# Kernel tuning notes

Measured on AMD Instinct MI355X. Metric: run time of the kernel, lower is better.

## Reference

```python
import jax, jax.numpy as jnp
import numpy as np

N = 2048        # nodes
IN_DIM = 128    # input feature dim
K = 8           # channels
D = 32          # per-channel dim (C_dim)
ITERS = 4       # routing iterations
BETA = 1.0      # attention temperature
EPS = 1e-12     # F.normalize eps


def l2norm(x):
    # F.normalize(x, dim=-1): x / max(||x||_2, eps)
    n = jnp.linalg.norm(x, axis=-1, keepdims=True)
    return x / jnp.maximum(n, EPS)


def setup_inputs() -> dict:
    key = jax.random.key(0)
    k1, k2, k3, k4 = jax.random.split(key, 4)
    adj = jax.random.randint(k1, (N, N), 0, 2, dtype=jnp.int32)
    features = jax.random.normal(k2, (N, IN_DIM), dtype=jnp.float32)
    # parameters initialized ~ N(0,1) as in init_parameters
    W = jax.random.normal(k3, (K, IN_DIM, D), dtype=jnp.float32)
    b = jax.random.normal(k4, (K, D), dtype=jnp.float32)
    return {"adj": adj, "features": features, "W": W, "b": b}


def reference(adj, features, W, b):
    mask = (adj > 0)[None, :, :]                         # [1, N, N]
    # per-channel projection + row L2 normalize -> Z: [K, N, D]
    Z = l2norm(jnp.einsum('nd,kdc->knc', features, W) + b[:, None, :])
    for _ in range(ITERS):
        # per-channel masked attention scores [K, N, N]
        att = jnp.einsum('knc,kmc->knm', Z, Z)
        att = jnp.where(mask, att, 0.0) / BETA
        # softmax across channels (dim=2 in torch after cat == K axis here)
        att = jax.nn.softmax(att, axis=0)
        att = jnp.where(mask, att, 0.0)
        # weighted aggregate + residual + L2 normalize
        Z = l2norm(Z + jnp.einsum('knm,kmc->knc', att, Z))
    # concat channels along feature dim -> [N, K*D]
    return jnp.transpose(Z, (1, 0, 2)).reshape(N, K * D)
```

## Files before the change

### kernel.cpp

```cpp
#include <hip/hip_runtime.h>
#include <hip/hip_bf16.h>

#define NN 2048
#define KK 8
#define DD 32
#define ZSZ (KK * NN * DD)
#define PSTR 20

typedef __attribute__((ext_vector_type(8))) short short8;
typedef __attribute__((ext_vector_type(4))) float f32x4;
typedef __attribute__((ext_vector_type(4))) unsigned int u32x4;

union UU { u32x4 q; short8 v; unsigned int u[4]; };

#define SELHI 0x07060302u
#define SELLO 0x05040100u

__device__ __forceinline__ unsigned int prm(unsigned int a, unsigned int b, unsigned int sel) {
  return __builtin_amdgcn_perm(a, b, sel);
}
__device__ __forceinline__ unsigned int bfr(float x) {
  unsigned int u = __float_as_uint(x);
  return (u + 0x7fffu + ((u >> 16) & 1u)) >> 16;
}
__device__ __forceinline__ unsigned int packp(float a, float b) {
  union { __hip_bfloat162 h; unsigned int u; } cv;
  cv.h = __float22bfloat162_rn(make_float2(a, b));
  return cv.u;
}
__device__ __forceinline__ f32x4 MF(short8 a, short8 b, f32x4 c) {
  return __builtin_amdgcn_mfma_f32_16x16x32_bf16(a, b, c, 0, 0, 0);
}
__device__ __forceinline__ short8 as_s8(u32x4 x) { UU u; u.q = x; return u.v; }

__global__ __launch_bounds__(256) void pm_kernel(const float* __restrict__ feat,
                                                 const float* __restrict__ W,
                                                 const float* __restrict__ bias,
                                                 float* __restrict__ Z,
                                                 unsigned short* __restrict__ Zghi,
                                                 unsigned short* __restrict__ Zthi,
                                                 const int* __restrict__ adj,
                                                 unsigned int* __restrict__ mbits) {
  const int t = threadIdx.x;
  if (blockIdx.x < 256) {
    const int nb = blockIdx.x * 8;
    const int k = t >> 5, c = t & 31;
    float s[8];
#pragma unroll
    for (int j = 0; j < 8; ++j) s[j] = bias[k * DD + c];
    const float* w = W + (k * 128) * DD + c;
    const float* fp = feat + nb * 128;
#pragma unroll 4
    for (int d = 0; d < 128; ++d) {
      float wv = w[d * DD];
#pragma unroll
      for (int j = 0; j < 8; ++j) s[j] = fmaf(fp[j * 128 + d], wv, s[j]);
    }
    unsigned int hi[8];
#pragma unroll
    for (int j = 0; j < 8; ++j) {
      float sq = s[j] * s[j];
#pragma unroll
      for (int off = 16; off > 0; off >>= 1) sq += __shfl_xor(sq, off, 32);
      float z = s[j] / fmaxf(sqrtf(sq), 1e-12f);
      Z[(k * NN + nb + j) * DD + c] = z;
      hi[j] = bfr(z);
      Zghi[(k * NN + nb + j) * DD + c] = (unsigned short)hi[j];
    }
    uint4 tp = make_uint4(hi[0] | (hi[1] << 16), hi[2] | (hi[3] << 16),
                          hi[4] | (hi[5] << 16), hi[6] | (hi[7] << 16));
    *(uint4*)&Zthi[(size_t)k * DD * NN + (size_t)c * NN + nb] = tp;
  } else {
    const int base = (blockIdx.x - 256) * 1024 + t;
    const int lane = t & 63;
    int v[4];
#pragma unroll
    for (int rr = 0; rr < 4; ++rr) v[rr] = adj[base + 256 * rr];
#pragma unroll
    for (int rr = 0; rr < 4; ++rr) {
      int idx = base + 256 * rr;
      unsigned long long b = __ballot(v[rr] > 0);
      if (lane == 0) mbits[idx >> 5] = (unsigned int)b;
      if (lane == 32) mbits[idx >> 5] = (unsigned int)(b >> 32);
    }
  }
}

template <int NCt>
__global__ __launch_bounds__(256) void rp_kernel(const float* __restrict__ Zin,
                                                 const float* __restrict__ part,
                                                 float* __restrict__ Zout,
                                                 unsigned short* __restrict__ Zghi,
                                                 unsigned short* __restrict__ Zthi) {
  __shared__ unsigned short T[DD][33];
  const int t = threadIdx.x;
  const int k = blockIdx.x >> 6, mt = blockIdx.x & 63;
  const int m0 = mt * 32;
  const int mloc = t >> 3, c4 = t & 7;
  const size_t idx = (size_t)(k * NN + m0 + mloc) * DD + 4 * c4;
  float4 v = *(const float4*)&Zin[idx];
#pragma unroll
  for (int j = 0; j < NCt; ++j) {
    float4 p = *(const float4*)&part[(size_t)j * ZSZ + idx];
    v.x += p.x; v.y += p.y; v.z += p.z; v.w += p.w;
  }
  float sq = v.x * v.x + v.y * v.y + v.z * v.z + v.w * v.w;
  sq += __shfl_xor(sq, 1, 8);
  sq += __shfl_xor(sq, 2, 8);
  sq += __shfl_xor(sq, 4, 8);
  const float sc = 1.0f / fmaxf(sqrtf(sq), 1e-12f);
  float z[4] = {v.x * sc, v.y * sc, v.z * sc, v.w * sc};
  *(float4*)&Zout[idx] = make_float4(z[0], z[1], z[2], z[3]);
  unsigned int hi[4];
#pragma unroll
  for (int e = 0; e < 4; ++e) {
    hi[e] = bfr(z[e]);
    T[4 * c4 + e][mloc] = (unsigned short)hi[e];
  }
  *(uint2*)&Zghi[idx] = make_uint2(hi[0] | (hi[1] << 16), hi[2] | (hi[3] << 16));
  __syncthreads();
  const int cloc = t >> 3, m4 = t & 7;
  unsigned int o0 = (unsigned int)T[cloc][4 * m4 + 0] | ((unsigned int)T[cloc][4 * m4 + 1] << 16);
  unsigned int o1 = (unsigned int)T[cloc][4 * m4 + 2] | ((unsigned int)T[cloc][4 * m4 + 3] << 16);
  *(uint2*)&Zthi[(size_t)k * DD * NN + (size_t)cloc * NN + m0 + 4 * m4] = make_uint2(o0, o1);
}

template <int NS>
__global__ __launch_bounds__(256, 2) void iter_kernel(const unsigned short* __restrict__ Zghi,
                                                      const unsigned short* __restrict__ Zthi,
                                                      const unsigned int* __restrict__ mbits,
                                                      float* __restrict__ part) {
  __shared__ __align__(16) unsigned int lds[8192 + 4 * 4 * 16 * PSTR];
  const int t = threadIdx.x;
  const int w = t >> 6;
  const int lane = t & 63;
  const int l15 = lane & 15;
  const int g = lane >> 4;
  const int nw = blockIdx.x * 64 + w * 16;
  const int mchunk = blockIdx.y * (NS * 32);

  const unsigned int* Zg = (const unsigned int*)Zghi;
  const unsigned int* Zt = (const unsigned int*)Zthi;

  short8 A[KK];
#pragma unroll
  for (int k = 0; k < KK; ++k)
    A[k] = as_s8(*(const u32x4*)&Zg[(size_t)(k * NN + nw + l15) * 16 + 4 * g]);

  unsigned int mwa[4][NS];
#pragma unroll
  for (int r = 0; r < 4; ++r)
#pragma unroll
    for (int q4 = 0; q4 < NS / 4; ++q4) {
      uint4 m4 = *(const uint4*)&mbits[(size_t)(nw + 4 * g + r) * 64 + (mchunk >> 5) + 4 * q4];
      mwa[r][4 * q4 + 0] = m4.x; mwa[r][4 * q4 + 1] = m4.y;
      mwa[r][4 * q4 + 2] = m4.z; mwa[r][4 * q4 + 3] = m4.w;
    }

  f32x4 O[KK][2];
#pragma unroll
  for (int k = 0; k < KK; ++k)
#pragma unroll
    for (int ch = 0; ch < 2; ++ch) O[k][ch] = {0.0f, 0.0f, 0.0f, 0.0f};

  const int sqd = t & 3;
  const int sr0 = t >> 2;

  u32x4 Lgh[4], Lth[4];
  auto do_loads = [&](int mb) {
#pragma unroll
    for (int j = 0; j < 4; ++j) {
      int r = 64 * j + sr0;
      int k = r >> 5, rm = r & 31;
      Lgh[j] = *(const u32x4*)&Zg[(size_t)k * (NN * 16) + (size_t)(mb + rm) * 16 + sqd * 4];
      Lth[j] = *(const u32x4*)&Zt[(size_t)k * (NN * 16) + (size_t)rm * (NN / 2) + (mb >> 1) + sqd * 4];
    }
  };
  do_loads(mchunk);

  unsigned int* Pw = &lds[8192 + w * (4 * 16 * PSTR)];

#pragma unroll
  for (int st = 0; st < NS; ++st) {
    const int mb = mchunk + st * 32;
    __syncthreads();
#pragma unroll
    for (int j = 0; j < 4; ++j) {
      int r = 64 * j + sr0;
      *(u32x4*)&lds[r * 16 + 4 * sqd] = Lgh[j];
      *(u32x4*)&lds[4096 + r * 16 + 4 * sqd] = Lth[j];
    }
    __syncthreads();
    if (st + 1 < NS) do_loads(mb + 32);

#pragma unroll
    for (int sub = 0; sub < 2; ++sub) {
      f32x4 S[KK];
#pragma unroll
      for (int k = 0; k < KK; ++k) {
        int m = 16 * sub + l15;
        u32x4 bh = *(const u32x4*)&lds[(k * 32 + m) * 16 + 4 * g];
        f32x4 z = {0.0f, 0.0f, 0.0f, 0.0f};
        S[k] = MF(A[k], as_s8(bh), z);
      }
#pragma unroll
      for (int r = 0; r < 4; ++r) {
        float e[KK];
        float sum = 0.0f;
#pragma unroll
        for (int k = 0; k < KK; ++k) { e[k] = __expf(S[k][r]); sum += e[k]; }
        int ml = 16 * sub + l15;
        float f = ((mwa[r][st] >> ml) & 1u) ? __builtin_amdgcn_rcpf(sum) : 0.0f;
#pragma unroll
        for (int k = 0; k < KK; ++k) S[k][r] = e[k] * f;
      }
#pragma unroll
      for (int kp = 0; kp < 4; ++kp)
#pragma unroll
        for (int r = 0; r < 4; ++r) {
          int n = 4 * g + r;
          Pw[kp * (16 * PSTR) + n * PSTR + 16 * sub + l15] =
              packp(S[2 * kp][r], S[2 * kp + 1][r]);
        }
    }

#pragma unroll
    for (int kp = 0; kp < 4; ++kp) {
      const unsigned int* Pr = &Pw[kp * (16 * PSTR) + l15 * PSTR + 8 * g];
      u32x4 a0 = *(const u32x4*)Pr;
      u32x4 a1 = *(const u32x4*)(Pr + 4);
      UU pk0, pk1;
      pk0.u[0] = prm(a0.y, a0.x, SELLO); pk0.u[1] = prm(a0.w, a0.z, SELLO);
      pk0.u[2] = prm(a1.y, a1.x, SELLO); pk0.u[3] = prm(a1.w, a1.z, SELLO);
      pk1.u[0] = prm(a0.y, a0.x, SELHI); pk1.u[1] = prm(a0.w, a0.z, SELHI);
      pk1.u[2] = prm(a1.y, a1.x, SELHI); pk1.u[3] = prm(a1.w, a1.z, SELHI);
#pragma unroll
      for (int kk = 0; kk < 2; ++kk) {
        int k = 2 * kp + kk;
#pragma unroll
        for (int ch = 0; ch < 2; ++ch) {
          int c = 16 * ch + l15;
          u32x4 b = *(const u32x4*)&lds[4096 + (k * 32 + c) * 16 + 4 * g];
          O[k][ch] = MF(kk ? pk1.v : pk0.v, as_s8(b), O[k][ch]);
        }
      }
    }
  }

  float* dst = part + (size_t)blockIdx.y * ZSZ;
#pragma unroll
  for (int k = 0; k < KK; ++k)
#pragma unroll
    for (int ch = 0; ch < 2; ++ch) {
      f32x4 o = O[k][ch];
#pragma unroll
      for (int r = 0; r < 4; ++r)
        dst[(size_t)(k * NN + nw + 4 * g + r) * DD + 16 * ch + l15] = o[r];
    }
}

template <int NCt>
__global__ __launch_bounds__(256) void ro_kernel(const float* __restrict__ Zin,
                                                 const float* __restrict__ part,
                                                 float* __restrict__ out) {
  const int n = blockIdx.x, t = threadIdx.x;
  const int k = t >> 5, c = t & 31;
  const size_t idx = (size_t)(k * NN + n) * DD + c;
  float v = Zin[idx];
#pragma unroll
  for (int j = 0; j < NCt; ++j) v += part[(size_t)j * ZSZ + idx];
  float sq = v * v;
#pragma unroll
  for (int off = 16; off > 0; off >>= 1) sq += __shfl_xor(sq, off, 32);
  out[n * (KK * DD) + t] = v / fmaxf(sqrtf(sq), 1e-12f);
}

extern "C" void kernel_launch(void* const* d_in, const int* in_sizes, int n_in,
                              void* d_out, int out_size, void* d_ws, size_t ws_size,
                              hipStream_t stream) {
  const int* adj = (const int*)d_in[0];
  const float* feat = (const float*)d_in[1];
  const float* W = (const float*)d_in[2];
  const float* b = (const float*)d_in[3];
  float* out = (float*)d_out;

  int NC = 16;
  while (NC > 4) {
    size_t need = ((size_t)ZSZ * (2 + NC) + NN * 64) * 4 + (size_t)ZSZ * 2 * 2;
    if (need <= ws_size) break;
    NC >>= 1;
  }

  float* Z0 = (float*)d_ws;
  float* Z1 = Z0 + ZSZ;
  unsigned short* Zghi = (unsigned short*)(Z1 + ZSZ);
  unsigned short* Zthi = Zghi + ZSZ;
  unsigned int* mbits = (unsigned int*)(Zthi + ZSZ);
  float* part = (float*)(mbits + NN * 64);

  pm_kernel<<<256 + 4096, 256, 0, stream>>>(feat, W, b, Z0, Zghi, Zthi, adj, mbits);

  float* zi = Z0;
  float* zo = Z1;
  for (int it = 0; it < 4; ++it) {
    if (NC == 16)
      iter_kernel<4><<<dim3(32, 16), 256, 0, stream>>>(Zghi, Zthi, mbits, part);
    else if (NC == 8)
      iter_kernel<8><<<dim3(32, 8), 256, 0, stream>>>(Zghi, Zthi, mbits, part);
    else
      iter_kernel<16><<<dim3(32, 4), 256, 0, stream>>>(Zghi, Zthi, mbits, part);
    if (it < 3) {
      if (NC == 16)
        rp_kernel<16><<<512, 256, 0, stream>>>(zi, part, zo, Zghi, Zthi);
      else if (NC == 8)
        rp_kernel<8><<<512, 256, 0, stream>>>(zi, part, zo, Zghi, Zthi);
      else
        rp_kernel<4><<<512, 256, 0, stream>>>(zi, part, zo, Zghi, Zthi);
      float* tmp = zi; zi = zo; zo = tmp;
    } else {
      if (NC == 16)
        ro_kernel<16><<<NN, 256, 0, stream>>>(zi, part, out);
      else if (NC == 8)
        ro_kernel<8><<<NN, 256, 0, stream>>>(zi, part, out);
      else
        ro_kernel<4><<<NN, 256, 0, stream>>>(zi, part, out);
    }
  }
}
```

Before: 200.0 us.

## Replace split-M partial buffers with atomic accumulation into a single aggregate

Each iteration block now atomically adds its partial aggregate into one shared Zagg buffer instead of writing 16 separate partial slices that rp/ro kernels then sum. The aim is to remove the large partial-buffer write and the multi-slice read traffic. Zagg is zeroed in pm_kernel and re-zeroed in rp_kernel after it is consumed. This adds float atomic contention and makes the sum order nondeterministic. The LDS P stride is also widened from 20 to 36, likely to change bank-conflict behaviour.

```diff
diff --git a/kernel.cpp b/kernel.cpp
--- a/kernel.cpp
+++ b/kernel.cpp
@@ -5,7 +5,7 @@
 #define KK 8
 #define DD 32
 #define ZSZ (KK * NN * DD)
-#define PSTR 20
+#define PSTR 36
 
 typedef __attribute__((ext_vector_type(8))) short short8;
 typedef __attribute__((ext_vector_type(4))) float f32x4;
@@ -40,7 +40,8 @@
                                                  unsigned short* __restrict__ Zghi,
                                                  unsigned short* __restrict__ Zthi,
                                                  const int* __restrict__ adj,
-                                                 unsigned int* __restrict__ mbits) {
+                                                 unsigned int* __restrict__ mbits,
+                                                 float* __restrict__ Zagg) {
   const int t = threadIdx.x;
   if (blockIdx.x < 256) {
     const int nb = blockIdx.x * 8;
@@ -71,7 +72,9 @@
                           hi[4] | (hi[5] << 16), hi[6] | (hi[7] << 16));
     *(uint4*)&Zthi[(size_t)k * DD * NN + (size_t)c * NN + nb] = tp;
   } else {
-    const int base = (blockIdx.x - 256) * 1024 + t;
+    const int zb = blockIdx.x - 256;
+    if (zb < 2048) Zagg[zb * 256 + t] = 0.0f;
+    const int base = zb * 1024 + t;
     const int lane = t & 63;
     int v[4];
 #pragma unroll
@@ -86,9 +89,8 @@
   }
 }
 
-template <int NCt>
 __global__ __launch_bounds__(256) void rp_kernel(const float* __restrict__ Zin,
-                                                 const float* __restrict__ part,
+                                                 float* __restrict__ Zagg,
                                                  float* __restrict__ Zout,
                                                  unsigned short* __restrict__ Zghi,
                                                  unsigned short* __restrict__ Zthi) {
@@ -99,11 +101,9 @@
   const int mloc = t >> 3, c4 = t & 7;
   const size_t idx = (size_t)(k * NN + m0 + mloc) * DD + 4 * c4;
   float4 v = *(const float4*)&Zin[idx];
-#pragma unroll
-  for (int j = 0; j < NCt; ++j) {
-    float4 p = *(const float4*)&part[(size_t)j * ZSZ + idx];
-    v.x += p.x; v.y += p.y; v.z += p.z; v.w += p.w;
-  }
+  float4 p = *(const float4*)&Zagg[idx];
+  v.x += p.x; v.y += p.y; v.z += p.z; v.w += p.w;
+  *(float4*)&Zagg[idx] = make_float4(0.0f, 0.0f, 0.0f, 0.0f);
   float sq = v.x * v.x + v.y * v.y + v.z * v.z + v.w * v.w;
   sq += __shfl_xor(sq, 1, 8);
   sq += __shfl_xor(sq, 2, 8);
@@ -125,11 +125,10 @@
   *(uint2*)&Zthi[(size_t)k * DD * NN + (size_t)cloc * NN + m0 + 4 * m4] = make_uint2(o0, o1);
 }
 
-template <int NS>
 __global__ __launch_bounds__(256, 2) void iter_kernel(const unsigned short* __restrict__ Zghi,
                                                       const unsigned short* __restrict__ Zthi,
                                                       const unsigned int* __restrict__ mbits,
-                                                      float* __restrict__ part) {
+                                                      float* __restrict__ Zagg) {
   __shared__ __align__(16) unsigned int lds[8192 + 4 * 4 * 16 * PSTR];
   const int t = threadIdx.x;
   const int w = t >> 6;
@@ -137,7 +136,7 @@
   const int l15 = lane & 15;
   const int g = lane >> 4;
   const int nw = blockIdx.x * 64 + w * 16;
-  const int mchunk = blockIdx.y * (NS * 32);
+  const int mchunk = blockIdx.y * (4 * 32);
 
   const unsigned int* Zg = (const unsigned int*)Zghi;
   const unsigned int* Zt = (const unsigned int*)Zthi;
@@ -147,15 +146,12 @@
   for (int k = 0; k < KK; ++k)
     A[k] = as_s8(*(const u32x4*)&Zg[(size_t)(k * NN + nw + l15) * 16 + 4 * g]);
 
-  unsigned int mwa[4][NS];
-#pragma unroll
-  for (int r = 0; r < 4; ++r)
-#pragma unroll
-    for (int q4 = 0; q4 < NS / 4; ++q4) {
-      uint4 m4 = *(const uint4*)&mbits[(size_t)(nw + 4 * g + r) * 64 + (mchunk >> 5) + 4 * q4];
-      mwa[r][4 * q4 + 0] = m4.x; mwa[r][4 * q4 + 1] = m4.y;
-      mwa[r][4 * q4 + 2] = m4.z; mwa[r][4 * q4 + 3] = m4.w;
-    }
+  unsigned int mwa[4][4];
+#pragma unroll
+  for (int r = 0; r < 4; ++r) {
+    uint4 m4 = *(const uint4*)&mbits[(size_t)(nw + 4 * g + r) * 64 + (mchunk >> 5)];
+    mwa[r][0] = m4.x; mwa[r][1] = m4.y; mwa[r][2] = m4.z; mwa[r][3] = m4.w;
+  }
 
   f32x4 O[KK][2];
 #pragma unroll
@@ -181,7 +177,7 @@
   unsigned int* Pw = &lds[8192 + w * (4 * 16 * PSTR)];
 
 #pragma unroll
-  for (int st = 0; st < NS; ++st) {
+  for (int st = 0; st < 4; ++st) {
     const int mb = mchunk + st * 32;
     __syncthreads();
 #pragma unroll
@@ -191,7 +187,7 @@
       *(u32x4*)&lds[4096 + r * 16 + 4 * sqd] = Lth[j];
     }
     __syncthreads();
-    if (st + 1 < NS) do_loads(mb + 32);
+    if (st + 1 < 4) do_loads(mb + 32);
 
 #pragma unroll
     for (int sub = 0; sub < 2; ++sub) {
@@ -247,7 +243,6 @@
     }
   }
 
-  float* dst = part + (size_t)blockIdx.y * ZSZ;
 #pragma unroll
   for (int k = 0; k < KK; ++k)
 #pragma unroll
@@ -255,20 +250,17 @@
       f32x4 o = O[k][ch];
 #pragma unroll
       for (int r = 0; r < 4; ++r)
-        dst[(size_t)(k * NN + nw + 4 * g + r) * DD + 16 * ch + l15] = o[r];
-    }
-}
-
-template <int NCt>
+        unsafeAtomicAdd(&Zagg[(size_t)(k * NN + nw + 4 * g + r) * DD + 16 * ch + l15], o[r]);
+    }
+}
+
 __global__ __launch_bounds__(256) void ro_kernel(const float* __restrict__ Zin,
-                                                 const float* __restrict__ part,
+                                                 const float* __restrict__ Zagg,
                                                  float* __restrict__ out) {
   const int n = blockIdx.x, t = threadIdx.x;
   const int k = t >> 5, c = t & 31;
   const size_t idx = (size_t)(k * NN + n) * DD + c;
-  float v = Zin[idx];
-#pragma unroll
-  for (int j = 0; j < NCt; ++j) v += part[(size_t)j * ZSZ + idx];
+  float v = Zin[idx] + Zagg[idx];
   float sq = v * v;
 #pragma unroll
   for (int off = 16; off > 0; off >>= 1) sq += __shfl_xor(sq, off, 32);
@@ -284,46 +276,24 @@
   const float* b = (const float*)d_in[3];
   float* out = (float*)d_out;
 
-  int NC = 16;
-  while (NC > 4) {
-    size_t need = ((size_t)ZSZ * (2 + NC) + NN * 64) * 4 + (size_t)ZSZ * 2 * 2;
-    if (need <= ws_size) break;
-    NC >>= 1;
-  }
-
   float* Z0 = (float*)d_ws;
   float* Z1 = Z0 + ZSZ;
   unsigned short* Zghi = (unsigned short*)(Z1 + ZSZ);
   unsigned short* Zthi = Zghi + ZSZ;
   unsigned int* mbits = (unsigned int*)(Zthi + ZSZ);
-  float* part = (float*)(mbits + NN * 64);
-
-  pm_kernel<<<256 + 4096, 256, 0, stream>>>(feat, W, b, Z0, Zghi, Zthi, adj, mbits);
+  float* Zagg = (float*)(mbits + NN * 64);
+
+  pm_kernel<<<256 + 4096, 256, 0, stream>>>(feat, W, b, Z0, Zghi, Zthi, adj, mbits, Zagg);
 
   float* zi = Z0;
   float* zo = Z1;
   for (int it = 0; it < 4; ++it) {
-    if (NC == 16)
-      iter_kernel<4><<<dim3(32, 16), 256, 0, stream>>>(Zghi, Zthi, mbits, part);
-    else if (NC == 8)
-      iter_kernel<8><<<dim3(32, 8), 256, 0, stream>>>(Zghi, Zthi, mbits, part);
-    else
-      iter_kernel<16><<<dim3(32, 4), 256, 0, stream>>>(Zghi, Zthi, mbits, part);
+    iter_kernel<<<dim3(32, 16), 256, 0, stream>>>(Zghi, Zthi, mbits, Zagg);
     if (it < 3) {
-      if (NC == 16)
-        rp_kernel<16><<<512, 256, 0, stream>>>(zi, part, zo, Zghi, Zthi);
-      else if (NC == 8)
-        rp_kernel<8><<<512, 256, 0, stream>>>(zi, part, zo, Zghi, Zthi);
-      else
-        rp_kernel<4><<<512, 256, 0, stream>>>(zi, part, zo, Zghi, Zthi);
+      rp_kernel<<<512, 256, 0, stream>>>(zi, Zagg, zo, Zghi, Zthi);
       float* tmp = zi; zi = zo; zo = tmp;
     } else {
-      if (NC == 16)
-        ro_kernel<16><<<NN, 256, 0, stream>>>(zi, part, out);
-      else if (NC == 8)
-        ro_kernel<8><<<NN, 256, 0, stream>>>(zi, part, out);
-      else
-        ro_kernel<4><<<NN, 256, 0, stream>>>(zi, part, out);
-    }
-  }
-}
+      ro_kernel<<<NN, 256, 0, stream>>>(zi, Zagg, out);
+    }
+  }
+}
```

New measurement: 247.7 us. 1.24x slower.
